# Kernel tuning notes

Measured on AMD Instinct MI355X. Metric: run time of the kernel, lower is better.

The kernel has to match this reference:

```python
import jax, jax.numpy as jnp
import numpy as np

N = 1_000_000      # total points
G = 256            # number of interaction clusters (segments)
D_IN = 4           # [energy, x, y, z] per-point features
H1, H2, LATENT = 64, 128, 256
D_OUT = 3          # vertex position dims


def setup_inputs() -> dict:
    key = jax.random.key(0)
    ks = jax.random.split(key, 10)
    point_cloud = jax.random.normal(ks[0], (N, 5), dtype=jnp.float32)
    seg_ids = jnp.sort(jax.random.randint(ks[1], (N,), 0, G, dtype=jnp.int64))
    def lin(k, fan_in, fan_out):
        s = 1.0 / np.sqrt(fan_in)
        return jax.random.uniform(k, (fan_in, fan_out), jnp.float32, -s, s)
    W1 = lin(ks[2], D_IN, H1);   b1 = jnp.zeros((H1,), jnp.float32)
    W2 = lin(ks[3], H1, H2);     b2 = jnp.zeros((H2,), jnp.float32)
    W3 = lin(ks[4], H2, LATENT); b3 = jnp.zeros((LATENT,), jnp.float32)
    Wf = lin(ks[5], LATENT, D_OUT); bf = jnp.zeros((D_OUT,), jnp.float32)
    return {"point_cloud": point_cloud, "W1": W1, "b1": b1, "W2": W2, "b2": b2,
            "W3": W3, "b3": b3, "Wf": Wf, "bf": bf, "seg_ids": seg_ids}


def reference(point_cloud, W1, b1, W2, b2, W3, b3, Wf, bf, seg_ids):
    pos = point_cloud[:, 1:4]          # [N,3]
    x = point_cloud[:, 4:5]            # [N,1] energy
    # --- per-segment centroids (segment mean, single pass) ---
    counts = jax.ops.segment_sum(jnp.ones((pos.shape[0],), pos.dtype), seg_ids,
                                 num_segments=G)                      # [G]
    centroids = jax.ops.segment_sum(pos, seg_ids, num_segments=G)
    centroids = centroids / jnp.maximum(counts, 1.0)[:, None]         # [G,3]
    # --- PointNet encoder: shared per-point MLP + per-segment max-pool ---
    feats = jnp.concatenate([x, pos], axis=1)                         # [N,4]
    h = jax.nn.relu(feats @ W1 + b1)                                  # [N,64]
    h = jax.nn.relu(h @ W2 + b2)                                      # [N,128]
    h = h @ W3 + b3                                                   # [N,256]
    pooled = jax.ops.segment_max(h, seg_ids, num_segments=G)          # [G,256]
    # --- final Linear + Softplus head, added to centroids ---
    out = jax.nn.softplus(pooled @ Wf + bf)                           # [G,3]
    return centroids + out
```

## Files before the change

kernel.cpp:

```cpp
#include <hip/hip_runtime.h>
#include <float.h>

typedef __bf16 bf16x8 __attribute__((ext_vector_type(8)));
typedef __bf16 bf16x4 __attribute__((ext_vector_type(4)));
typedef float  f32x4  __attribute__((ext_vector_type(4)));

#define G      256
#define MT     32
#define H1DIM  64
#define H2DIM  128
#define LAT    256
#define H1PAD  72
#define H2PAD  136

__device__ __forceinline__ unsigned mapf(float f) {
  unsigned u = __float_as_uint(f);
  return (u & 0x80000000u) ? ~u : (u | 0x80000000u);
}
__device__ __forceinline__ float unmapf(unsigned u) {
  return (u & 0x80000000u) ? __uint_as_float(u & 0x7fffffffu) : __uint_as_float(~u);
}

__device__ __forceinline__ void flush4(f32x4 v0, f32x4 v1, f32x4 v2, f32x4 v3,
                                       int s, int w, int q, int nn,
                                       const float* __restrict__ b3,
                                       unsigned* __restrict__ pooled) {
  f32x4 vv[4] = {v0, v1, v2, v3};
  #pragma unroll
  for (int mt = 0; mt < 4; ++mt)
    #pragma unroll
    for (int r = 0; r < 4; ++r) {
      int feat = w * 64 + mt * 16 + q * 4 + r;
      float v = vv[mt][r] + b3[feat];
      v = fmaxf(v, __shfl_xor(v, 1));
      v = fmaxf(v, __shfl_xor(v, 2));
      v = fmaxf(v, __shfl_xor(v, 4));
      v = fmaxf(v, __shfl_xor(v, 8));
      if (nn == 0) atomicMax(&pooled[s * LAT + feat], mapf(v));
    }
}

__global__ __launch_bounds__(256, 2) void mlp_kernel(
    const float* __restrict__ pc,
    const float* __restrict__ W1, const float* __restrict__ b1,
    const float* __restrict__ W2, const float* __restrict__ b2,
    const float* __restrict__ W3, const float* __restrict__ b3,
    const int* __restrict__ sid,
    unsigned* __restrict__ pooled,
    float* __restrict__ sums,
    int n, int tiles_per_block) {
  __shared__ __align__(16) __bf16 shF[MT][8];
  __shared__ __align__(16) __bf16 sh1[MT][H1PAD];
  __shared__ __align__(16) __bf16 sh2[MT][H2PAD];
  __shared__ int segt[MT];

  const int t  = threadIdx.x;
  const int w  = t >> 6;
  const int lane = t & 63;
  const int q  = lane >> 4;
  const int nn = lane & 15;

  bf16x8 w1f;
  #pragma unroll
  for (int j = 0; j < 8; ++j) {
    int k = q * 8 + j;
    w1f[j] = (k < 4) ? (__bf16)W1[k * H1DIM + w * 16 + nn] : (__bf16)0.f;
  }
  float b1r[4];
  #pragma unroll
  for (int r = 0; r < 4; ++r) b1r[r] = b1[w * 16 + q * 4 + r];

  bf16x8 w2f[2][2];
  float  b2r[2][4];
  #pragma unroll
  for (int mt = 0; mt < 2; ++mt) {
    int m = w * 32 + mt * 16 + nn;
    #pragma unroll
    for (int ks = 0; ks < 2; ++ks)
      #pragma unroll
      for (int j = 0; j < 8; ++j)
        w2f[mt][ks][j] = (__bf16)W2[(ks * 32 + q * 8 + j) * H2DIM + m];
    #pragma unroll
    for (int r = 0; r < 4; ++r) b2r[mt][r] = b2[w * 32 + mt * 16 + q * 4 + r];
  }

  bf16x8 w3f[4][4];
  #pragma unroll
  for (int mt = 0; mt < 4; ++mt) {
    int m = w * 64 + mt * 16 + nn;
    #pragma unroll
    for (int ks = 0; ks < 4; ++ks)
      #pragma unroll
      for (int j = 0; j < 8; ++j)
        w3f[mt][ks][j] = (__bf16)W3[(ks * 32 + q * 8 + j) * LAT + m];
  }

  const f32x4 zero4 = {0.f, 0.f, 0.f, 0.f};
  const bf16x8 zero8 = {};
  const f32x4 neginf4 = {-FLT_MAX, -FLT_MAX, -FLT_MAX, -FLT_MAX};

  f32x4 run[4];
  #pragma unroll
  for (int mt = 0; mt < 4; ++mt) run[mt] = neginf4;

  float cx = 0.f, cy = 0.f, cz = 0.f, cc = 0.f;
  int   cseg = -1;

  const int tile0 = blockIdx.x * tiles_per_block;
  int first = tile0 * MT; if (first > n - 1) first = n - 1;
  int s_cur = sid[first];

  for (int ti = 0; ti < tiles_per_block; ++ti) {
    const int base = (tile0 + ti) * MT;
    if (base >= n) break;

    if (t < MT) {
      int p = base + t;
      bool valid = p < n;
      int pcl = valid ? p : (n - 1);
      const float* pp = pc + (size_t)pcl * 5;
      float fx = pp[4], p1 = pp[1], p2 = pp[2], p3 = pp[3];
      bf16x8 v = {};
      v[0] = (__bf16)fx;
      v[1] = (__bf16)p1;
      v[2] = (__bf16)p2;
      v[3] = (__bf16)p3;
      *reinterpret_cast<bf16x8*>(&shF[t][0]) = v;
      int s = sid[pcl];
      segt[t] = s;
      if (valid) {
        if (s != cseg) {
          if (cc > 0.f) {
            atomicAdd(&sums[cseg * 4 + 0], cx);
            atomicAdd(&sums[cseg * 4 + 1], cy);
            atomicAdd(&sums[cseg * 4 + 2], cz);
            atomicAdd(&sums[cseg * 4 + 3], cc);
          }
          cseg = s; cx = 0.f; cy = 0.f; cz = 0.f; cc = 0.f;
        }
        cx += p1; cy += p2; cz += p3; cc += 1.f;
      }
    }
    __syncthreads();

    {
      f32x4 acc1[2];
      #pragma unroll
      for (int nt = 0; nt < 2; ++nt) {
        bf16x8 ld = *reinterpret_cast<const bf16x8*>(&shF[nt * 16 + nn][0]);
        bf16x8 af = (q == 0) ? ld : zero8;
        acc1[nt] = __builtin_amdgcn_mfma_f32_16x16x32_bf16(w1f, af, zero4, 0, 0, 0);
      }
      #pragma unroll
      for (int nt = 0; nt < 2; ++nt) {
        bf16x4 pk;
        #pragma unroll
        for (int r = 0; r < 4; ++r)
          pk[r] = (__bf16)fmaxf(acc1[nt][r] + b1r[r], 0.f);
        *reinterpret_cast<bf16x4*>(&sh1[nt * 16 + nn][w * 16 + q * 4]) = pk;
      }
    }
    __syncthreads();

    {
      f32x4 acc2[2][2];
      #pragma unroll
      for (int mt = 0; mt < 2; ++mt)
        #pragma unroll
        for (int nt = 0; nt < 2; ++nt) acc2[mt][nt] = zero4;
      #pragma unroll
      for (int ks = 0; ks < 2; ++ks) {
        bf16x8 bfr[2];
        #pragma unroll
        for (int nt = 0; nt < 2; ++nt)
          bfr[nt] = *reinterpret_cast<const bf16x8*>(&sh1[nt * 16 + nn][ks * 32 + q * 8]);
        #pragma unroll
        for (int mt = 0; mt < 2; ++mt)
          #pragma unroll
          for (int nt = 0; nt < 2; ++nt)
            acc2[mt][nt] = __builtin_amdgcn_mfma_f32_16x16x32_bf16(w2f[mt][ks], bfr[nt], acc2[mt][nt], 0, 0, 0);
      }
      #pragma unroll
      for (int mt = 0; mt < 2; ++mt)
        #pragma unroll
        for (int nt = 0; nt < 2; ++nt) {
          bf16x4 pk;
          #pragma unroll
          for (int r = 0; r < 4; ++r)
            pk[r] = (__bf16)fmaxf(acc2[mt][nt][r] + b2r[mt][r], 0.f);
          *reinterpret_cast<bf16x4*>(&sh2[nt * 16 + nn][w * 32 + mt * 16 + q * 4]) = pk;
        }
    }
    __syncthreads();

    f32x4 acc3[4][2];
    #pragma unroll
    for (int mt = 0; mt < 4; ++mt)
      #pragma unroll
      for (int nt = 0; nt < 2; ++nt) acc3[mt][nt] = zero4;
    #pragma unroll
    for (int ks = 0; ks < 4; ++ks) {
      bf16x8 bfr[2];
      #pragma unroll
      for (int nt = 0; nt < 2; ++nt)
        bfr[nt] = *reinterpret_cast<const bf16x8*>(&sh2[nt * 16 + nn][ks * 32 + q * 8]);
      #pragma unroll
      for (int mt = 0; mt < 4; ++mt)
        #pragma unroll
        for (int nt = 0; nt < 2; ++nt)
          acc3[mt][nt] = __builtin_amdgcn_mfma_f32_16x16x32_bf16(w3f[mt][ks], bfr[nt], acc3[mt][nt], 0, 0, 0);
    }

    int smin = segt[0], smax = segt[MT - 1];
    if (smin != s_cur) {
      flush4(run[0], run[1], run[2], run[3], s_cur, w, q, nn, b3, pooled);
      #pragma unroll
      for (int mt = 0; mt < 4; ++mt) run[mt] = neginf4;
      s_cur = smin;
    }
    if (smin == smax) {
      #pragma unroll
      for (int mt = 0; mt < 4; ++mt)
        #pragma unroll
        for (int r = 0; r < 4; ++r)
          run[mt][r] = fmaxf(run[mt][r], fmaxf(acc3[mt][0][r], acc3[mt][1][r]));
    } else {
      int sg0 = segt[nn], sg1 = segt[16 + nn];
      for (int s = smin; s <= smax; ++s) {
        f32x4 tmp[4];
        #pragma unroll
        for (int mt = 0; mt < 4; ++mt)
          #pragma unroll
          for (int r = 0; r < 4; ++r) {
            float v0 = (sg0 == s) ? acc3[mt][0][r] : -FLT_MAX;
            float v1 = (sg1 == s) ? acc3[mt][1][r] : -FLT_MAX;
            tmp[mt][r] = fmaxf(v0, v1);
          }
        if (s < smax) {
          if (s == s_cur) {
            #pragma unroll
            for (int mt = 0; mt < 4; ++mt)
              #pragma unroll
              for (int r = 0; r < 4; ++r) run[mt][r] = fmaxf(run[mt][r], tmp[mt][r]);
            flush4(run[0], run[1], run[2], run[3], s, w, q, nn, b3, pooled);
            #pragma unroll
            for (int mt = 0; mt < 4; ++mt) run[mt] = neginf4;
          } else {
            flush4(tmp[0], tmp[1], tmp[2], tmp[3], s, w, q, nn, b3, pooled);
          }
        } else {
          #pragma unroll
          for (int mt = 0; mt < 4; ++mt)
            #pragma unroll
            for (int r = 0; r < 4; ++r) run[mt][r] = fmaxf(run[mt][r], tmp[mt][r]);
        }
      }
      s_cur = smax;
    }
    __syncthreads();
  }
  flush4(run[0], run[1], run[2], run[3], s_cur, w, q, nn, b3, pooled);

  if (t < MT && cc > 0.f) {
    atomicAdd(&sums[cseg * 4 + 0], cx);
    atomicAdd(&sums[cseg * 4 + 1], cy);
    atomicAdd(&sums[cseg * 4 + 2], cz);
    atomicAdd(&sums[cseg * 4 + 3], cc);
  }
}

__global__ void final_kernel(const float* __restrict__ sums, const unsigned* __restrict__ pooled,
                             const float* __restrict__ Wf, const float* __restrict__ bfv,
                             float* __restrict__ out) {
  __shared__ float red[4][3];
  int g = blockIdx.x;
  int t = threadIdx.x;
  unsigned u = pooled[g * LAT + t];
  float f = u ? unmapf(u) : 0.f;
  float s0 = f * Wf[t * 3 + 0];
  float s1 = f * Wf[t * 3 + 1];
  float s2 = f * Wf[t * 3 + 2];
  #pragma unroll
  for (int off = 1; off < 64; off <<= 1) {
    s0 += __shfl_xor(s0, off);
    s1 += __shfl_xor(s1, off);
    s2 += __shfl_xor(s2, off);
  }
  int wave = t >> 6;
  if ((t & 63) == 0) { red[wave][0] = s0; red[wave][1] = s1; red[wave][2] = s2; }
  __syncthreads();
  if (t < 3) {
    float acc = bfv[t] + red[0][t] + red[1][t] + red[2][t] + red[3][t];
    float sp  = fmaxf(acc, 0.f) + log1pf(expf(-fabsf(acc)));
    float cnt = fmaxf(sums[g * 4 + 3], 1.f);
    float cen = sums[g * 4 + t] / cnt;
    out[g * 3 + t] = cen + sp;
  }
}

extern "C" void kernel_launch(void* const* d_in, const int* in_sizes, int n_in,
                              void* d_out, int out_size, void* d_ws, size_t ws_size,
                              hipStream_t stream) {
  const float* pc  = (const float*)d_in[0];
  const float* W1  = (const float*)d_in[1];
  const float* b1  = (const float*)d_in[2];
  const float* W2  = (const float*)d_in[3];
  const float* b2  = (const float*)d_in[4];
  const float* W3  = (const float*)d_in[5];
  const float* b3  = (const float*)d_in[6];
  const float* Wf  = (const float*)d_in[7];
  const float* bfv = (const float*)d_in[8];
  const int*   sid = (const int*)d_in[9];
  int n = in_sizes[0] / 5;

  float*    sums   = (float*)d_ws;
  unsigned* pooled = (unsigned*)((char*)d_ws + 4096);
  hipMemsetAsync(d_ws, 0, 4096 + (size_t)G * LAT * 4, stream);

  int tiles   = (n + MT - 1) / MT;
  int nblocks = 512;
  int tpb     = (tiles + nblocks - 1) / nblocks;
  mlp_kernel<<<nblocks, 256, 0, stream>>>(pc, W1, b1, W2, b2, W3, b3, sid, pooled, sums, n, tpb);

  final_kernel<<<G, 256, 0, stream>>>(sums, pooled, Wf, bfv, (float*)d_out);
}
```

Before: 220.2 us.

## Split MLP across eight waves and prefetch next tile's points into registers

Doubles the block to 512 threads (8 waves), so each wave computes half as many output rows per layer: 16 rows of layer 2 and 32 features of layer 3. Layer 1 runs only on the upper four waves. This halves per-wave weight registers and MFMA work per tile, aiming at more parallelism and occupancy. The next tile's point coordinates and segment id are also loaded into registers ahead of time to hide global load latency. The cost is more waves taking part in each block barrier, and half the waves sit idle during layer 1.

```diff
diff --git a/kernel.cpp b/kernel.cpp
--- a/kernel.cpp
+++ b/kernel.cpp
@@ -21,16 +21,16 @@
   return (u & 0x80000000u) ? __uint_as_float(u & 0x7fffffffu) : __uint_as_float(~u);
 }
 
-__device__ __forceinline__ void flush4(f32x4 v0, f32x4 v1, f32x4 v2, f32x4 v3,
+__device__ __forceinline__ void flush2(f32x4 v0, f32x4 v1,
                                        int s, int w, int q, int nn,
                                        const float* __restrict__ b3,
                                        unsigned* __restrict__ pooled) {
-  f32x4 vv[4] = {v0, v1, v2, v3};
+  f32x4 vv[2] = {v0, v1};
   #pragma unroll
-  for (int mt = 0; mt < 4; ++mt)
+  for (int mt = 0; mt < 2; ++mt)
     #pragma unroll
     for (int r = 0; r < 4; ++r) {
-      int feat = w * 64 + mt * 16 + q * 4 + r;
+      int feat = w * 32 + mt * 16 + q * 4 + r;
       float v = vv[mt][r] + b3[feat];
       v = fmaxf(v, __shfl_xor(v, 1));
       v = fmaxf(v, __shfl_xor(v, 2));
@@ -40,7 +40,7 @@
     }
 }
 
-__global__ __launch_bounds__(256, 2) void mlp_kernel(
+__global__ __launch_bounds__(512, 4) void mlp_kernel(
     const float* __restrict__ pc,
     const float* __restrict__ W1, const float* __restrict__ b1,
     const float* __restrict__ W2, const float* __restrict__ b2,
@@ -60,35 +60,37 @@
   const int q  = lane >> 4;
   const int nn = lane & 15;
 
-  bf16x8 w1f;
-  #pragma unroll
-  for (int j = 0; j < 8; ++j) {
-    int k = q * 8 + j;
-    w1f[j] = (k < 4) ? (__bf16)W1[k * H1DIM + w * 16 + nn] : (__bf16)0.f;
-  }
-  float b1r[4];
-  #pragma unroll
-  for (int r = 0; r < 4; ++r) b1r[r] = b1[w * 16 + q * 4 + r];
-
-  bf16x8 w2f[2][2];
-  float  b2r[2][4];
+  bf16x8 w1f = {};
+  float b1r[4] = {0.f, 0.f, 0.f, 0.f};
+  if (w >= 4) {
+    int wl = w - 4;
+    #pragma unroll
+    for (int j = 0; j < 8; ++j) {
+      int k = q * 8 + j;
+      w1f[j] = (k < 4) ? (__bf16)W1[k * H1DIM + wl * 16 + nn] : (__bf16)0.f;
+    }
+    #pragma unroll
+    for (int r = 0; r < 4; ++r) b1r[r] = b1[wl * 16 + q * 4 + r];
+  }
+
+  bf16x8 w2f[2];
+  float  b2r[4];
+  {
+    int m = w * 16 + nn;
+    #pragma unroll
+    for (int ks = 0; ks < 2; ++ks)
+      #pragma unroll
+      for (int j = 0; j < 8; ++j)
+        w2f[ks][j] = (__bf16)W2[(ks * 32 + q * 8 + j) * H2DIM + m];
+    #pragma unroll
+    for (int r = 0; r < 4; ++r) b2r[r] = b2[w * 16 + q * 4 + r];
+  }
+
+  bf16x8 w3f[2][4];
   #pragma unroll
   for (int mt = 0; mt < 2; ++mt) {
     int m = w * 32 + mt * 16 + nn;
     #pragma unroll
-    for (int ks = 0; ks < 2; ++ks)
-      #pragma unroll
-      for (int j = 0; j < 8; ++j)
-        w2f[mt][ks][j] = (__bf16)W2[(ks * 32 + q * 8 + j) * H2DIM + m];
-    #pragma unroll
-    for (int r = 0; r < 4; ++r) b2r[mt][r] = b2[w * 32 + mt * 16 + q * 4 + r];
-  }
-
-  bf16x8 w3f[4][4];
-  #pragma unroll
-  for (int mt = 0; mt < 4; ++mt) {
-    int m = w * 64 + mt * 16 + nn;
-    #pragma unroll
     for (int ks = 0; ks < 4; ++ks)
       #pragma unroll
       for (int j = 0; j < 8; ++j)
@@ -99,9 +101,8 @@
   const bf16x8 zero8 = {};
   const f32x4 neginf4 = {-FLT_MAX, -FLT_MAX, -FLT_MAX, -FLT_MAX};
 
-  f32x4 run[4];
-  #pragma unroll
-  for (int mt = 0; mt < 4; ++mt) run[mt] = neginf4;
+  f32x4 run[2];
+  run[0] = neginf4; run[1] = neginf4;
 
   float cx = 0.f, cy = 0.f, cz = 0.f, cc = 0.f;
   int   cseg = -1;
@@ -110,40 +111,55 @@
   int first = tile0 * MT; if (first > n - 1) first = n - 1;
   int s_cur = sid[first];
 
+  float pf1 = 0.f, pf2 = 0.f, pf3 = 0.f, pfx = 0.f;
+  int   pfs = 0; bool pfv = false;
+  if (t < MT) {
+    int p = tile0 * MT + t;
+    pfv = p < n;
+    int pcl = pfv ? p : (n - 1);
+    const float* pp = pc + (size_t)pcl * 5;
+    pf1 = pp[1]; pf2 = pp[2]; pf3 = pp[3]; pfx = pp[4];
+    pfs = sid[pcl];
+  }
+
   for (int ti = 0; ti < tiles_per_block; ++ti) {
     const int base = (tile0 + ti) * MT;
     if (base >= n) break;
 
     if (t < MT) {
-      int p = base + t;
-      bool valid = p < n;
-      int pcl = valid ? p : (n - 1);
-      const float* pp = pc + (size_t)pcl * 5;
-      float fx = pp[4], p1 = pp[1], p2 = pp[2], p3 = pp[3];
       bf16x8 v = {};
-      v[0] = (__bf16)fx;
-      v[1] = (__bf16)p1;
-      v[2] = (__bf16)p2;
-      v[3] = (__bf16)p3;
+      v[0] = (__bf16)pfx;
+      v[1] = (__bf16)pf1;
+      v[2] = (__bf16)pf2;
+      v[3] = (__bf16)pf3;
       *reinterpret_cast<bf16x8*>(&shF[t][0]) = v;
-      int s = sid[pcl];
-      segt[t] = s;
-      if (valid) {
-        if (s != cseg) {
+      segt[t] = pfs;
+      if (pfv) {
+        if (pfs != cseg) {
           if (cc > 0.f) {
             atomicAdd(&sums[cseg * 4 + 0], cx);
             atomicAdd(&sums[cseg * 4 + 1], cy);
             atomicAdd(&sums[cseg * 4 + 2], cz);
             atomicAdd(&sums[cseg * 4 + 3], cc);
           }
-          cseg = s; cx = 0.f; cy = 0.f; cz = 0.f; cc = 0.f;
+          cseg = pfs; cx = 0.f; cy = 0.f; cz = 0.f; cc = 0.f;
         }
-        cx += p1; cy += p2; cz += p3; cc += 1.f;
+        cx += pf1; cy += pf2; cz += pf3; cc += 1.f;
       }
     }
     __syncthreads();
 
-    {
+    if (t < MT) {
+      int p = (tile0 + ti + 1) * MT + t;
+      pfv = p < n;
+      int pcl = pfv ? p : (n - 1);
+      const float* pp = pc + (size_t)pcl * 5;
+      pf1 = pp[1]; pf2 = pp[2]; pf3 = pp[3]; pfx = pp[4];
+      pfs = sid[pcl];
+    }
+
+    if (w >= 4) {
+      int wl = w - 4;
       f32x4 acc1[2];
       #pragma unroll
       for (int nt = 0; nt < 2; ++nt) {
@@ -157,17 +173,14 @@
         #pragma unroll
         for (int r = 0; r < 4; ++r)
           pk[r] = (__bf16)fmaxf(acc1[nt][r] + b1r[r], 0.f);
-        *reinterpret_cast<bf16x4*>(&sh1[nt * 16 + nn][w * 16 + q * 4]) = pk;
+        *reinterpret_cast<bf16x4*>(&sh1[nt * 16 + nn][wl * 16 + q * 4]) = pk;
       }
     }
     __syncthreads();
 
     {
-      f32x4 acc2[2][2];
-      #pragma unroll
-      for (int mt = 0; mt < 2; ++mt)
-        #pragma unroll
-        for (int nt = 0; nt < 2; ++nt) acc2[mt][nt] = zero4;
+      f32x4 acc2[2];
+      acc2[0] = zero4; acc2[1] = zero4;
       #pragma unroll
       for (int ks = 0; ks < 2; ++ks) {
         bf16x8 bfr[2];
@@ -175,27 +188,23 @@
         for (int nt = 0; nt < 2; ++nt)
           bfr[nt] = *reinterpret_cast<const bf16x8*>(&sh1[nt * 16 + nn][ks * 32 + q * 8]);
         #pragma unroll
-        for (int mt = 0; mt < 2; ++mt)
-          #pragma unroll
-          for (int nt = 0; nt < 2; ++nt)
-            acc2[mt][nt] = __builtin_amdgcn_mfma_f32_16x16x32_bf16(w2f[mt][ks], bfr[nt], acc2[mt][nt], 0, 0, 0);
-      }
-      #pragma unroll
-      for (int mt = 0; mt < 2; ++mt)
-        #pragma unroll
-        for (int nt = 0; nt < 2; ++nt) {
-          bf16x4 pk;
-          #pragma unroll
-          for (int r = 0; r < 4; ++r)
-            pk[r] = (__bf16)fmaxf(acc2[mt][nt][r] + b2r[mt][r], 0.f);
-          *reinterpret_cast<bf16x4*>(&sh2[nt * 16 + nn][w * 32 + mt * 16 + q * 4]) = pk;
-        }
+        for (int nt = 0; nt < 2; ++nt)
+          acc2[nt] = __builtin_amdgcn_mfma_f32_16x16x32_bf16(w2f[ks], bfr[nt], acc2[nt], 0, 0, 0);
+      }
+      #pragma unroll
+      for (int nt = 0; nt < 2; ++nt) {
+        bf16x4 pk;
+        #pragma unroll
+        for (int r = 0; r < 4; ++r)
+          pk[r] = (__bf16)fmaxf(acc2[nt][r] + b2r[r], 0.f);
+        *reinterpret_cast<bf16x4*>(&sh2[nt * 16 + nn][w * 16 + q * 4]) = pk;
+      }
     }
     __syncthreads();
 
-    f32x4 acc3[4][2];
-    #pragma unroll
-    for (int mt = 0; mt < 4; ++mt)
+    f32x4 acc3[2][2];
+    #pragma unroll
+    for (int mt = 0; mt < 2; ++mt)
       #pragma unroll
       for (int nt = 0; nt < 2; ++nt) acc3[mt][nt] = zero4;
     #pragma unroll
@@ -205,7 +214,7 @@
       for (int nt = 0; nt < 2; ++nt)
         bfr[nt] = *reinterpret_cast<const bf16x8*>(&sh2[nt * 16 + nn][ks * 32 + q * 8]);
       #pragma unroll
-      for (int mt = 0; mt < 4; ++mt)
+      for (int mt = 0; mt < 2; ++mt)
         #pragma unroll
         for (int nt = 0; nt < 2; ++nt)
           acc3[mt][nt] = __builtin_amdgcn_mfma_f32_16x16x32_bf16(w3f[mt][ks], bfr[nt], acc3[mt][nt], 0, 0, 0);
@@ -213,23 +222,22 @@
 
     int smin = segt[0], smax = segt[MT - 1];
     if (smin != s_cur) {
-      flush4(run[0], run[1], run[2], run[3], s_cur, w, q, nn, b3, pooled);
-      #pragma unroll
-      for (int mt = 0; mt < 4; ++mt) run[mt] = neginf4;
+      flush2(run[0], run[1], s_cur, w, q, nn, b3, pooled);
+      run[0] = neginf4; run[1] = neginf4;
       s_cur = smin;
     }
     if (smin == smax) {
       #pragma unroll
-      for (int mt = 0; mt < 4; ++mt)
+      for (int mt = 0; mt < 2; ++mt)
         #pragma unroll
         for (int r = 0; r < 4; ++r)
           run[mt][r] = fmaxf(run[mt][r], fmaxf(acc3[mt][0][r], acc3[mt][1][r]));
     } else {
       int sg0 = segt[nn], sg1 = segt[16 + nn];
       for (int s = smin; s <= smax; ++s) {
-        f32x4 tmp[4];
-        #pragma unroll
-        for (int mt = 0; mt < 4; ++mt)
+        f32x4 tmp[2];
+        #pragma unroll
+        for (int mt = 0; mt < 2; ++mt)
           #pragma unroll
           for (int r = 0; r < 4; ++r) {
             float v0 = (sg0 == s) ? acc3[mt][0][r] : -FLT_MAX;
@@ -239,18 +247,17 @@
         if (s < smax) {
           if (s == s_cur) {
             #pragma unroll
-            for (int mt = 0; mt < 4; ++mt)
+            for (int mt = 0; mt < 2; ++mt)
               #pragma unroll
               for (int r = 0; r < 4; ++r) run[mt][r] = fmaxf(run[mt][r], tmp[mt][r]);
-            flush4(run[0], run[1], run[2], run[3], s, w, q, nn, b3, pooled);
-            #pragma unroll
-            for (int mt = 0; mt < 4; ++mt) run[mt] = neginf4;
+            flush2(run[0], run[1], s, w, q, nn, b3, pooled);
+            run[0] = neginf4; run[1] = neginf4;
           } else {
-            flush4(tmp[0], tmp[1], tmp[2], tmp[3], s, w, q, nn, b3, pooled);
+            flush2(tmp[0], tmp[1], s, w, q, nn, b3, pooled);
           }
         } else {
           #pragma unroll
-          for (int mt = 0; mt < 4; ++mt)
+          for (int mt = 0; mt < 2; ++mt)
             #pragma unroll
             for (int r = 0; r < 4; ++r) run[mt][r] = fmaxf(run[mt][r], tmp[mt][r]);
         }
@@ -259,7 +266,7 @@
     }
     __syncthreads();
   }
-  flush4(run[0], run[1], run[2], run[3], s_cur, w, q, nn, b3, pooled);
+  flush2(run[0], run[1], s_cur, w, q, nn, b3, pooled);
 
   if (t < MT && cc > 0.f) {
     atomicAdd(&sums[cseg * 4 + 0], cx);
@@ -320,7 +327,7 @@
   int tiles   = (n + MT - 1) / MT;
   int nblocks = 512;
   int tpb     = (tiles + nblocks - 1) / nblocks;
-  mlp_kernel<<<nblocks, 256, 0, stream>>>(pc, W1, b1, W2, b2, W3, b3, sid, pooled, sums, n, tpb);
+  mlp_kernel<<<nblocks, 512, 0, stream>>>(pc, W1, b1, W2, b2, W3, b3, sid, pooled, sums, n, tpb);
 
   final_kernel<<<G, 256, 0, stream>>>(sums, pooled, Wf, bfv, (float*)d_out);
 }
```

Result: no change. 222.1 us (+0.8%).

## Double tile size with 512-thread blocks, prefetch next tile inputs, pipeline LDS loads

Applied to the files above, without the earlier changes.

Doubles the point tile to 64 and block size to 512 threads, where pairs of waves share a feature group and split the points, halving the block count. Wave 0 prefetches the next tile's point features and segment ids into registers during compute. Layer-3 LDS fragment loads are software-pipelined, and __syncthreads is replaced by a waitcnt+s_barrier helper. The aim is to hide global load latency and cut per-tile barrier overhead, at the cost of weights now being replicated across two waves per feature group, which raises register pressure, and of fewer blocks in flight.

```diff
diff --git a/kernel.cpp b/kernel.cpp
--- a/kernel.cpp
+++ b/kernel.cpp
@@ -6,13 +6,19 @@
 typedef float  f32x4  __attribute__((ext_vector_type(4)));
 
 #define G      256
-#define MT     32
+#define MT     64
 #define H1DIM  64
 #define H2DIM  128
 #define LAT    256
 #define H1PAD  72
 #define H2PAD  136
 
+__device__ __forceinline__ void barrier_lgkm() {
+  asm volatile("s_waitcnt lgkmcnt(0)" ::: "memory");
+  __builtin_amdgcn_s_barrier();
+  asm volatile("" ::: "memory");
+}
+
 __device__ __forceinline__ unsigned mapf(float f) {
   unsigned u = __float_as_uint(f);
   return (u & 0x80000000u) ? ~u : (u | 0x80000000u);
@@ -22,7 +28,7 @@
 }
 
 __device__ __forceinline__ void flush4(f32x4 v0, f32x4 v1, f32x4 v2, f32x4 v3,
-                                       int s, int w, int q, int nn,
+                                       int s, int fg, int q, int nn,
                                        const float* __restrict__ b3,
                                        unsigned* __restrict__ pooled) {
   f32x4 vv[4] = {v0, v1, v2, v3};
@@ -30,7 +36,7 @@
   for (int mt = 0; mt < 4; ++mt)
     #pragma unroll
     for (int r = 0; r < 4; ++r) {
-      int feat = w * 64 + mt * 16 + q * 4 + r;
+      int feat = fg * 64 + mt * 16 + q * 4 + r;
       float v = vv[mt][r] + b3[feat];
       v = fmaxf(v, __shfl_xor(v, 1));
       v = fmaxf(v, __shfl_xor(v, 2));
@@ -40,7 +46,7 @@
     }
 }
 
-__global__ __launch_bounds__(256, 2) void mlp_kernel(
+__global__ __launch_bounds__(512, 2) void mlp_kernel(
     const float* __restrict__ pc,
     const float* __restrict__ W1, const float* __restrict__ b1,
     const float* __restrict__ W2, const float* __restrict__ b2,
@@ -54,40 +60,42 @@
   __shared__ __align__(16) __bf16 sh2[MT][H2PAD];
   __shared__ int segt[MT];
 
-  const int t  = threadIdx.x;
-  const int w  = t >> 6;
+  const int t    = threadIdx.x;
+  const int w    = t >> 6;
+  const int fg   = w >> 1;
+  const int pg   = w & 1;
   const int lane = t & 63;
-  const int q  = lane >> 4;
-  const int nn = lane & 15;
+  const int q    = lane >> 4;
+  const int nn   = lane & 15;
 
   bf16x8 w1f;
   #pragma unroll
   for (int j = 0; j < 8; ++j) {
     int k = q * 8 + j;
-    w1f[j] = (k < 4) ? (__bf16)W1[k * H1DIM + w * 16 + nn] : (__bf16)0.f;
+    w1f[j] = (k < 4) ? (__bf16)W1[k * H1DIM + fg * 16 + nn] : (__bf16)0.f;
   }
   float b1r[4];
   #pragma unroll
-  for (int r = 0; r < 4; ++r) b1r[r] = b1[w * 16 + q * 4 + r];
+  for (int r = 0; r < 4; ++r) b1r[r] = b1[fg * 16 + q * 4 + r];
 
   bf16x8 w2f[2][2];
   float  b2r[2][4];
   #pragma unroll
   for (int mt = 0; mt < 2; ++mt) {
-    int m = w * 32 + mt * 16 + nn;
+    int m = fg * 32 + mt * 16 + nn;
     #pragma unroll
     for (int ks = 0; ks < 2; ++ks)
       #pragma unroll
       for (int j = 0; j < 8; ++j)
         w2f[mt][ks][j] = (__bf16)W2[(ks * 32 + q * 8 + j) * H2DIM + m];
     #pragma unroll
-    for (int r = 0; r < 4; ++r) b2r[mt][r] = b2[w * 32 + mt * 16 + q * 4 + r];
+    for (int r = 0; r < 4; ++r) b2r[mt][r] = b2[fg * 32 + mt * 16 + q * 4 + r];
   }
 
   bf16x8 w3f[4][4];
   #pragma unroll
   for (int mt = 0; mt < 4; ++mt) {
-    int m = w * 64 + mt * 16 + nn;
+    int m = fg * 64 + mt * 16 + nn;
     #pragma unroll
     for (int ks = 0; ks < 4; ++ks)
       #pragma unroll
@@ -110,110 +118,131 @@
   int first = tile0 * MT; if (first > n - 1) first = n - 1;
   int s_cur = sid[first];
 
+  float pf1 = 0.f, pf2 = 0.f, pf3 = 0.f, pfx = 0.f;
+  int   pfs = 0; bool pfv = false;
+  if (w == 0) {
+    int p = tile0 * MT + lane;
+    pfv = p < n;
+    int pcl = pfv ? p : (n - 1);
+    const float* pp = pc + (size_t)pcl * 5;
+    pf1 = pp[1]; pf2 = pp[2]; pf3 = pp[3]; pfx = pp[4];
+    pfs = sid[pcl];
+  }
+
   for (int ti = 0; ti < tiles_per_block; ++ti) {
     const int base = (tile0 + ti) * MT;
     if (base >= n) break;
 
-    if (t < MT) {
-      int p = base + t;
-      bool valid = p < n;
-      int pcl = valid ? p : (n - 1);
-      const float* pp = pc + (size_t)pcl * 5;
-      float fx = pp[4], p1 = pp[1], p2 = pp[2], p3 = pp[3];
+    if (w == 0) {
       bf16x8 v = {};
-      v[0] = (__bf16)fx;
-      v[1] = (__bf16)p1;
-      v[2] = (__bf16)p2;
-      v[3] = (__bf16)p3;
-      *reinterpret_cast<bf16x8*>(&shF[t][0]) = v;
-      int s = sid[pcl];
-      segt[t] = s;
-      if (valid) {
-        if (s != cseg) {
+      v[0] = (__bf16)pfx;
+      v[1] = (__bf16)pf1;
+      v[2] = (__bf16)pf2;
+      v[3] = (__bf16)pf3;
+      *reinterpret_cast<bf16x8*>(&shF[lane][0]) = v;
+      segt[lane] = pfs;
+      if (pfv) {
+        if (pfs != cseg) {
           if (cc > 0.f) {
             atomicAdd(&sums[cseg * 4 + 0], cx);
             atomicAdd(&sums[cseg * 4 + 1], cy);
             atomicAdd(&sums[cseg * 4 + 2], cz);
             atomicAdd(&sums[cseg * 4 + 3], cc);
           }
-          cseg = s; cx = 0.f; cy = 0.f; cz = 0.f; cc = 0.f;
-        }
-        cx += p1; cy += p2; cz += p3; cc += 1.f;
-      }
-    }
-    __syncthreads();
+          cseg = pfs; cx = 0.f; cy = 0.f; cz = 0.f; cc = 0.f;
+        }
+        cx += pf1; cy += pf2; cz += pf3; cc += 1.f;
+      }
+    }
+    barrier_lgkm();
+
+    if (w == 0) {
+      int p = (tile0 + ti + 1) * MT + lane;
+      pfv = p < n;
+      int pcl = pfv ? p : (n - 1);
+      const float* pp = pc + (size_t)pcl * 5;
+      pf1 = pp[1]; pf2 = pp[2]; pf3 = pp[3]; pfx = pp[4];
+      pfs = sid[pcl];
+    }
 
     {
       f32x4 acc1[2];
       #pragma unroll
-      for (int nt = 0; nt < 2; ++nt) {
-        bf16x8 ld = *reinterpret_cast<const bf16x8*>(&shF[nt * 16 + nn][0]);
+      for (int c = 0; c < 2; ++c) {
+        bf16x8 ld = *reinterpret_cast<const bf16x8*>(&shF[pg * 32 + c * 16 + nn][0]);
         bf16x8 af = (q == 0) ? ld : zero8;
-        acc1[nt] = __builtin_amdgcn_mfma_f32_16x16x32_bf16(w1f, af, zero4, 0, 0, 0);
-      }
-      #pragma unroll
-      for (int nt = 0; nt < 2; ++nt) {
+        acc1[c] = __builtin_amdgcn_mfma_f32_16x16x32_bf16(w1f, af, zero4, 0, 0, 0);
+      }
+      #pragma unroll
+      for (int c = 0; c < 2; ++c) {
         bf16x4 pk;
         #pragma unroll
         for (int r = 0; r < 4; ++r)
-          pk[r] = (__bf16)fmaxf(acc1[nt][r] + b1r[r], 0.f);
-        *reinterpret_cast<bf16x4*>(&sh1[nt * 16 + nn][w * 16 + q * 4]) = pk;
-      }
-    }
-    __syncthreads();
+          pk[r] = (__bf16)fmaxf(acc1[c][r] + b1r[r], 0.f);
+        *reinterpret_cast<bf16x4*>(&sh1[pg * 32 + c * 16 + nn][fg * 16 + q * 4]) = pk;
+      }
+    }
+    barrier_lgkm();
 
     {
+      bf16x8 f2[2][2];
+      #pragma unroll
+      for (int ks = 0; ks < 2; ++ks)
+        #pragma unroll
+        for (int c = 0; c < 2; ++c)
+          f2[ks][c] = *reinterpret_cast<const bf16x8*>(&sh1[pg * 32 + c * 16 + nn][ks * 32 + q * 8]);
       f32x4 acc2[2][2];
       #pragma unroll
       for (int mt = 0; mt < 2; ++mt)
         #pragma unroll
-        for (int nt = 0; nt < 2; ++nt) acc2[mt][nt] = zero4;
-      #pragma unroll
-      for (int ks = 0; ks < 2; ++ks) {
-        bf16x8 bfr[2];
-        #pragma unroll
-        for (int nt = 0; nt < 2; ++nt)
-          bfr[nt] = *reinterpret_cast<const bf16x8*>(&sh1[nt * 16 + nn][ks * 32 + q * 8]);
+        for (int c = 0; c < 2; ++c) acc2[mt][c] = zero4;
+      #pragma unroll
+      for (int ks = 0; ks < 2; ++ks)
         #pragma unroll
         for (int mt = 0; mt < 2; ++mt)
           #pragma unroll
-          for (int nt = 0; nt < 2; ++nt)
-            acc2[mt][nt] = __builtin_amdgcn_mfma_f32_16x16x32_bf16(w2f[mt][ks], bfr[nt], acc2[mt][nt], 0, 0, 0);
-      }
+          for (int c = 0; c < 2; ++c)
+            acc2[mt][c] = __builtin_amdgcn_mfma_f32_16x16x32_bf16(w2f[mt][ks], f2[ks][c], acc2[mt][c], 0, 0, 0);
       #pragma unroll
       for (int mt = 0; mt < 2; ++mt)
         #pragma unroll
-        for (int nt = 0; nt < 2; ++nt) {
+        for (int c = 0; c < 2; ++c) {
           bf16x4 pk;
           #pragma unroll
           for (int r = 0; r < 4; ++r)
-            pk[r] = (__bf16)fmaxf(acc2[mt][nt][r] + b2r[mt][r], 0.f);
-          *reinterpret_cast<bf16x4*>(&sh2[nt * 16 + nn][w * 32 + mt * 16 + q * 4]) = pk;
-        }
-    }
-    __syncthreads();
+            pk[r] = (__bf16)fmaxf(acc2[mt][c][r] + b2r[mt][r], 0.f);
+          *reinterpret_cast<bf16x4*>(&sh2[pg * 32 + c * 16 + nn][fg * 32 + mt * 16 + q * 4]) = pk;
+        }
+    }
+    barrier_lgkm();
 
     f32x4 acc3[4][2];
     #pragma unroll
     for (int mt = 0; mt < 4; ++mt)
       #pragma unroll
-      for (int nt = 0; nt < 2; ++nt) acc3[mt][nt] = zero4;
-    #pragma unroll
-    for (int ks = 0; ks < 4; ++ks) {
-      bf16x8 bfr[2];
-      #pragma unroll
-      for (int nt = 0; nt < 2; ++nt)
-        bfr[nt] = *reinterpret_cast<const bf16x8*>(&sh2[nt * 16 + nn][ks * 32 + q * 8]);
-      #pragma unroll
-      for (int mt = 0; mt < 4; ++mt)
-        #pragma unroll
-        for (int nt = 0; nt < 2; ++nt)
-          acc3[mt][nt] = __builtin_amdgcn_mfma_f32_16x16x32_bf16(w3f[mt][ks], bfr[nt], acc3[mt][nt], 0, 0, 0);
+      for (int c = 0; c < 2; ++c) acc3[mt][c] = zero4;
+    {
+      bf16x8 fA0 = *reinterpret_cast<const bf16x8*>(&sh2[pg * 32 + 0 * 16 + nn][0 * 32 + q * 8]);
+      bf16x8 fA1 = *reinterpret_cast<const bf16x8*>(&sh2[pg * 32 + 1 * 16 + nn][0 * 32 + q * 8]);
+      #pragma unroll
+      for (int ks = 0; ks < 4; ++ks) {
+        bf16x8 nB0, nB1;
+        if (ks < 3) {
+          nB0 = *reinterpret_cast<const bf16x8*>(&sh2[pg * 32 + 0 * 16 + nn][(ks + 1) * 32 + q * 8]);
+          nB1 = *reinterpret_cast<const bf16x8*>(&sh2[pg * 32 + 1 * 16 + nn][(ks + 1) * 32 + q * 8]);
+        }
+        #pragma unroll
+        for (int mt = 0; mt < 4; ++mt) {
+          acc3[mt][0] = __builtin_amdgcn_mfma_f32_16x16x32_bf16(w3f[mt][ks], fA0, acc3[mt][0], 0, 0, 0);
+          acc3[mt][1] = __builtin_amdgcn_mfma_f32_16x16x32_bf16(w3f[mt][ks], fA1, acc3[mt][1], 0, 0, 0);
+        }
+        fA0 = nB0; fA1 = nB1;
+      }
     }
 
     int smin = segt[0], smax = segt[MT - 1];
     if (smin != s_cur) {
-      flush4(run[0], run[1], run[2], run[3], s_cur, w, q, nn, b3, pooled);
+      flush4(run[0], run[1], run[2], run[3], s_cur, fg, q, nn, b3, pooled);
       #pragma unroll
       for (int mt = 0; mt < 4; ++mt) run[mt] = neginf4;
       s_cur = smin;
@@ -225,7 +254,7 @@
         for (int r = 0; r < 4; ++r)
           run[mt][r] = fmaxf(run[mt][r], fmaxf(acc3[mt][0][r], acc3[mt][1][r]));
     } else {
-      int sg0 = segt[nn], sg1 = segt[16 + nn];
+      int sg0 = segt[pg * 32 + nn], sg1 = segt[pg * 32 + 16 + nn];
       for (int s = smin; s <= smax; ++s) {
         f32x4 tmp[4];
         #pragma unroll
@@ -242,11 +271,11 @@
             for (int mt = 0; mt < 4; ++mt)
               #pragma unroll
               for (int r = 0; r < 4; ++r) run[mt][r] = fmaxf(run[mt][r], tmp[mt][r]);
-            flush4(run[0], run[1], run[2], run[3], s, w, q, nn, b3, pooled);
+            flush4(run[0], run[1], run[2], run[3], s, fg, q, nn, b3, pooled);
             #pragma unroll
             for (int mt = 0; mt < 4; ++mt) run[mt] = neginf4;
           } else {
-            flush4(tmp[0], tmp[1], tmp[2], tmp[3], s, w, q, nn, b3, pooled);
+            flush4(tmp[0], tmp[1], tmp[2], tmp[3], s, fg, q, nn, b3, pooled);
           }
         } else {
           #pragma unroll
@@ -257,11 +286,11 @@
       }
       s_cur = smax;
     }
-    __syncthreads();
-  }
-  flush4(run[0], run[1], run[2], run[3], s_cur, w, q, nn, b3, pooled);
-
-  if (t < MT && cc > 0.f) {
+    barrier_lgkm();
+  }
+  flush4(run[0], run[1], run[2], run[3], s_cur, fg, q, nn, b3, pooled);
+
+  if (w == 0 && cc > 0.f) {
     atomicAdd(&sums[cseg * 4 + 0], cx);
     atomicAdd(&sums[cseg * 4 + 1], cy);
     atomicAdd(&sums[cseg * 4 + 2], cz);
@@ -318,9 +347,9 @@
   hipMemsetAsync(d_ws, 0, 4096 + (size_t)G * LAT * 4, stream);
 
   int tiles   = (n + MT - 1) / MT;
-  int nblocks = 512;
+  int nblocks = 256;
   int tpb     = (tiles + nblocks - 1) / nblocks;
-  mlp_kernel<<<nblocks, 256, 0, stream>>>(pc, W1, b1, W2, b2, W3, b3, sid, pooled, sums, n, tpb);
+  mlp_kernel<<<nblocks, 512, 0, stream>>>(pc, W1, b1, W2, b2, W3, b3, sid, pooled, sums, n, tpb);
 
   final_kernel<<<G, 256, 0, stream>>>(sums, pooled, Wf, bfv, (float*)d_out);
 }
```

Result: slower. 233.3 us (+6.0%).
